# Optimization experiments

Measured on AMD Instinct MI355X. Metric: run time of the kernel, lower is better.

## Reference

```python
import jax, jax.numpy as jnp
import numpy as np

B, N, E = 256, 512, 8192
F_IN, DEPTH, NHID = 128, 3, 256
CAT = F_IN + DEPTH * NHID  # 896


def setup_inputs() -> dict:
    key = jax.random.key(0)
    ks = jax.random.split(key, 20)
    def w(k, shape, fan_in):
        return jax.random.normal(k, shape, jnp.float32) / np.sqrt(fan_in)
    inp = {
        "x": jax.random.normal(ks[0], (B, N, F_IN), jnp.float32),
        "edge_index": jax.random.randint(ks[1], (2, E), 0, N, jnp.int64),
        # linears: first maps F_IN->NHID, rest NHID->NHID (stacked)
        "lin0_W": w(ks[2], (F_IN, NHID), F_IN),
        "lin0_b": jnp.zeros((NHID,), jnp.float32),
        "lin_Ws": w(ks[3], (DEPTH - 1, NHID, NHID), NHID),
        "lin_bs": jnp.zeros((DEPTH - 1, NHID), jnp.float32),
        # GCNConv weights (stacked), PyG semantics: A_norm (X W) + b
        "conv_Ws": w(ks[4], (DEPTH, NHID, NHID), NHID),
        "conv_bs": jnp.zeros((DEPTH, NHID), jnp.float32),
        "sig_W": w(ks[5], (CAT, NHID), CAT),
        "sig_b": jnp.zeros((NHID,), jnp.float32),
        "tanh_W": w(ks[6], (CAT, NHID), CAT),
        "tanh_b": jnp.zeros((NHID,), jnp.float32),
        "f1_W": w(ks[7], (NHID, NHID), NHID),
        "f1_b": jnp.zeros((NHID,), jnp.float32),
        "f2_W": w(ks[8], (NHID, 2), NHID),
        "f2_b": jnp.zeros((2,), jnp.float32),
    }
    return inp


def _gcn_norm(edge_index, n):
    # add self loops, compute symmetric normalization D^-1/2 (A+I) D^-1/2
    loop = jnp.arange(n, dtype=edge_index.dtype)
    src = jnp.concatenate([edge_index[0], loop])
    dst = jnp.concatenate([edge_index[1], loop])
    deg = jax.ops.segment_sum(jnp.ones_like(src, jnp.float32), dst, num_segments=n)
    dinv = jax.lax.rsqrt(jnp.maximum(deg, 1.0))
    norm = dinv[src] * dinv[dst]  # [E+N]
    return src, dst, norm


def _gcn(h, W, b, src, dst, norm, n):
    # h: [B, N, C]
    hW = h @ W
    msg = hW[:, src, :] * norm[None, :, None]          # [B, E+N, C]
    agg = jax.vmap(lambda m: jax.ops.segment_sum(m, dst, num_segments=n))(msg)
    return agg + b


def reference(x, edge_index, lin0_W, lin0_b, lin_Ws, lin_bs, conv_Ws, conv_bs,
              sig_W, sig_b, tanh_W, tanh_b, f1_W, f1_b, f2_W, f2_b):
    n = x.shape[1]
    src, dst, norm = _gcn_norm(edge_index, n)
    xs = [x]
    out = x
    for i in range(DEPTH):
        if i == 0:
            out = out @ lin0_W + lin0_b
        else:
            out = out @ lin_Ws[i - 1] + lin_bs[i - 1]
        out = _gcn(out, conv_Ws[i], conv_bs[i], src, dst, norm, n)
        out = jnp.tanh(out)
        xs.append(out)
    cat = jnp.concatenate(xs, axis=-1)                 # [B, N, CAT]
    s = jax.nn.sigmoid(cat @ sig_W + sig_b)            # [B, N, NHID]
    t = jnp.tanh(cat @ tanh_W + tanh_b)                # [B, N, NHID]
    pooled = jnp.sum(s * t, axis=1)                    # [B, NHID] (sum over nodes)
    embeds = jnp.tanh(pooled)
    h = jax.nn.relu(embeds @ f1_W + f1_b)              # dropout is eval-mode identity
    preds = h @ f2_W + f2_b                            # [B, 2]
    preds = jnp.concatenate([jax.nn.sigmoid(preds[:, :1]), preds[:, 1:]], axis=-1)
    return preds, embeds
```

## Files before the change

### kernel.cpp

```cpp
#include <hip/hip_runtime.h>
#include <hip/hip_bf16.h>
#include <cstdint>

typedef _Float16 half_t;
typedef __attribute__((ext_vector_type(8))) _Float16 half8;
typedef __attribute__((ext_vector_type(4))) _Float16 half4;
typedef __attribute__((ext_vector_type(4))) float f32x4;

#define MFMA16x32(a, b, c) __builtin_amdgcn_mfma_f32_16x16x32_f16(a, b, c, 0, 0, 0)

static constexpr int NB  = 256;
static constexpr int NN  = 512;
static constexpr int NE  = 8192;
static constexpr int FIN = 128;
static constexpr int NH  = 256;
static constexpr int CAT = 896;

__device__ __forceinline__ void xcd_swz(int& bx, int& by)
{
    const int nwg = gridDim.x * gridDim.y;
    int wgid = blockIdx.y * gridDim.x + blockIdx.x;
    wgid = (wgid & 7) * (nwg >> 3) + (wgid >> 3);
    bx = wgid % gridDim.x;
    by = wgid / gridDim.x;
}

__device__ __forceinline__ void gload16(const half_t* __restrict__ g, half_t* l)
{
    __builtin_amdgcn_global_load_lds(
        (const __attribute__((address_space(1))) uint32_t*)(uintptr_t)g,
        (__attribute__((address_space(3))) uint32_t*)(uintptr_t)l, 16, 0, 0);
}

__device__ __forceinline__ void stage128x64(
    const half_t* __restrict__ src, long row0, int ldk, int k0,
    half_t* lds, int tid)
{
    const int wid = tid >> 6, lane = tid & 63;
#pragma unroll
    for (int it = 0; it < 4; ++it) {
        const int rb   = wid * 32 + it * 8;
        const int row  = rb + (lane >> 3);
        const int slot = (lane & 7) ^ (row & 7);
        gload16(src + (row0 + row) * (long)ldk + k0 + slot * 8,
                lds + (size_t)rb * 64);
    }
}

__device__ __forceinline__ half8 fragr(const half_t* lds, int row, int slot)
{
    return *(const half8*)(lds + row * 64 + ((slot ^ (row & 7)) * 8));
}

struct Tab {
    const void* src[16];
    float*      dst[16];
    int         n[16];
    int         fi[16];
    int         nseg;
};

__global__ void k_detect_all(Tab t, int* __restrict__ flags)
{
    const int s = blockIdx.x;
    if (s >= t.nseg) return;
    __shared__ int cnt_s;
    if (threadIdx.x == 0) cnt_s = 0;
    __syncthreads();
    const uint32_t* w = (const uint32_t*)t.src[s];
    int nw = t.n[s] / 2; if (nw > 2048) nw = 2048; if (nw < 1) nw = 1;
    int c = 0;
    for (int i = threadIdx.x; i < nw; i += 256) {
        const uint32_t lo = w[i] & 0xFFFFu;
        const int e = (int)((lo >> 7) & 0xFF);
        if (lo == 0u || (e >= 116 && e <= 136)) ++c;
    }
    atomicAdd(&cnt_s, c);
    __syncthreads();
    if (threadIdx.x == 0) flags[t.fi[s]] = (2 * cnt_s >= nw) ? 1 : 0;
}

__global__ void k_cvt_all(Tab t, const int* __restrict__ flags)
{
    for (int s = 0; s < t.nseg; ++s) {
        float* dst = t.dst[s];
        if (dst == nullptr) continue;
        const int is_bf = flags[t.fi[s]];
        const int n = t.n[s];
        const void* src = t.src[s];
        for (int i = blockIdx.x * 256 + threadIdx.x; i < n; i += gridDim.x * 256)
            dst[i] = is_bf
                ? __uint_as_float(((uint32_t)((const uint16_t*)src)[i]) << 16)
                : ((const float*)src)[i];
    }
}

__global__ void k_x2h(const void* __restrict__ xraw, half_t* __restrict__ o,
                      size_t n8, const int* __restrict__ flag)
{
    const int is_bf = *flag;
    const size_t gid0 = (size_t)blockIdx.x * blockDim.x + threadIdx.x;
    const size_t stride = (size_t)gridDim.x * blockDim.x;
    if (is_bf) {
        const uint4* src = (const uint4*)xraw;
        for (size_t i = gid0; i < n8; i += stride) {
            const uint4 v = src[i];
            half8 h;
            h[0] = (_Float16)__uint_as_float((v.x & 0xFFFFu) << 16);
            h[1] = (_Float16)__uint_as_float(v.x & 0xFFFF0000u);
            h[2] = (_Float16)__uint_as_float((v.y & 0xFFFFu) << 16);
            h[3] = (_Float16)__uint_as_float(v.y & 0xFFFF0000u);
            h[4] = (_Float16)__uint_as_float((v.z & 0xFFFFu) << 16);
            h[5] = (_Float16)__uint_as_float(v.z & 0xFFFF0000u);
            h[6] = (_Float16)__uint_as_float((v.w & 0xFFFFu) << 16);
            h[7] = (_Float16)__uint_as_float(v.w & 0xFFFF0000u);
            ((half8*)o)[i] = h;
        }
    } else {
        const float4* src = (const float4*)xraw;
        for (size_t i = gid0; i < n8; i += stride) {
            const float4 a = src[2 * i], b = src[2 * i + 1];
            half8 h;
            h[0] = (_Float16)a.x; h[1] = (_Float16)a.y;
            h[2] = (_Float16)a.z; h[3] = (_Float16)a.w;
            h[4] = (_Float16)b.x; h[5] = (_Float16)b.y;
            h[6] = (_Float16)b.z; h[7] = (_Float16)b.w;
            ((half8*)o)[i] = h;
        }
    }
}

__global__ void k_sentinel(__hip_bfloat16* __restrict__ out, float code)
{
    const int i = blockIdx.x * 256 + threadIdx.x;
    if (i < 66048) out[i] = __float2bfloat16(i < 512 ? code : 0.f);
}

__global__ void k_pick512(const float* __restrict__ a, const float* __restrict__ b,
                          float* __restrict__ f2Wc, float* __restrict__ linbsc)
{
    __shared__ float sa_s, sb_s;
    const int t = threadIdx.x;
    if (t == 0) { sa_s = 0.f; sb_s = 0.f; }
    __syncthreads();
    float va = fabsf(a[t]) + fabsf(a[t + 256]);
    float vb = fabsf(b[t]) + fabsf(b[t + 256]);
    for (int o = 32; o; o >>= 1) {
        va += __shfl_down(va, o, 64);
        vb += __shfl_down(vb, o, 64);
    }
    if ((t & 63) == 0) { atomicAdd(&sa_s, va); atomicAdd(&sb_s, vb); }
    __syncthreads();
    const float* f2 = (sa_s >= sb_s) ? a : b;
    const float* lb = (sa_s >= sb_s) ? b : a;
    f2Wc[t] = f2[t]; f2Wc[t + 256] = f2[t + 256];
    linbsc[t] = lb[t]; linbsc[t + 256] = lb[t + 256];
}

__global__ void k_build_graph(const int* __restrict__ ei, int* __restrict__ rowptr,
                              int* __restrict__ colx, float* __restrict__ wn,
                              float* __restrict__ srow)
{
    __shared__ int   degs[NN];
    __shared__ float dinv[NN];
    __shared__ int   rp[NN + 1];
    __shared__ int   cur[NN];
    __shared__ float sacc[NN];
    __shared__ int   is64_s;
    const int t = threadIdx.x;
    degs[t] = 0; cur[t] = 0; sacc[t] = 0.f;
    if (t == 0) {
        int orv = 0;
        for (int i = 1; i < 256; i += 2) orv |= ei[i];
        is64_s = (orv == 0) ? 1 : 0;
    }
    __syncthreads();
    const bool is64 = (is64_s != 0);
    auto EV = [&](int idx) { return is64 ? ei[2 * idx] : ei[idx]; };

    for (int e = t; e < NE; e += NN)
        atomicAdd(&degs[EV(NE + e)], 1);
    __syncthreads();
    const float dv = rsqrtf(fmaxf((float)(degs[t] + 1), 1.f));
    dinv[t] = dv;
    __syncthreads();
    if (t == 0) {
        rp[0] = 0;
        for (int i = 0; i < NN; ++i) rp[i + 1] = rp[i] + degs[i] + 1;
    }
    __syncthreads();
    rowptr[t] = rp[t];
    if (t == 0) rowptr[NN] = rp[NN];
    for (int e = t; e < NE; e += NN) {
        const int s = EV(e), d = EV(NE + e);
        const int pos = atomicAdd(&cur[d], 1);
        colx[rp[d] + pos] = s;
        wn[rp[d] + pos]   = dinv[s] * dinv[d];
        atomicAdd(&sacc[d], dinv[s]);
    }
    __syncthreads();
    const int slot = rp[t + 1] - 1;
    colx[slot] = t;
    wn[slot]   = dv * dv;
    srow[t]    = dv * (sacc[t] + dv);
}

__global__ void k_densify(const int* __restrict__ rowptr, const int* __restrict__ colx,
                          const float* __restrict__ wn, half_t* __restrict__ S16)
{
    __shared__ float row[NN];
    const int d = blockIdx.x;
    for (int i = threadIdx.x; i < NN; i += 256) row[i] = 0.f;
    __syncthreads();
    const int s0 = rowptr[d], s1 = rowptr[d + 1];
    for (int e = s0 + threadIdx.x; e < s1; e += 256)
        atomicAdd(&row[colx[e]], wn[e]);
    __syncthreads();
    for (int i = threadIdx.x; i < NN; i += 256)
        S16[(size_t)d * NN + i] = (half_t)row[i];
}

__global__ void k_fold_wc(const float* __restrict__ lin0_W, const float* __restrict__ lin_Ws,
                          const float* __restrict__ conv_Ws,
                          half_t* __restrict__ wc0, half_t* __restrict__ wc1,
                          half_t* __restrict__ wc2)
{
    const int layer = blockIdx.y;
    const int k = blockIdx.x;
    const int n = threadIdx.x;
    const int K = (layer == 0) ? FIN : NH;
    if (k >= K) return;
    const float* lin = (layer == 0) ? lin0_W : lin_Ws + (size_t)(layer - 1) * NH * NH;
    const float* cw  = conv_Ws + (size_t)layer * NH * NH;
    float s = 0.f;
    for (int j = 0; j < NH; ++j) s += lin[k * NH + j] * cw[j * NH + n];
    half_t* o = (layer == 0) ? wc0 : ((layer == 1) ? wc1 : wc2);
    o[n * K + k] = (half_t)s;
}

__global__ void k_fold_wt(const float* __restrict__ sigW, const float* __restrict__ tanW,
                          half_t* __restrict__ sh, half_t* __restrict__ th,
                          const float* __restrict__ lin0_b, const float* __restrict__ lin_bs,
                          const float* __restrict__ conv_Ws, float* __restrict__ vb)
{
    const int which = blockIdx.y;
    if (which == 2) {
        const int layer = blockIdx.x;
        if (layer >= 3) return;
        const int n = threadIdx.x;
        const float* lb = (layer == 0) ? lin0_b : lin_bs + (size_t)(layer - 1) * NH;
        const float* cw = conv_Ws + (size_t)layer * NH * NH;
        float s = 0.f;
        for (int j = 0; j < NH; ++j) s += lb[j] * cw[j * NH + n];
        vb[layer * NH + n] = s;
        return;
    }
    const int n = blockIdx.x;
    const float* W = which ? tanW : sigW;
    half_t* o = which ? th : sh;
    for (int k = threadIdx.x; k < CAT; k += 256)
        o[(size_t)n * CAT + k] = (half_t)W[(size_t)k * NH + n];
}

__global__ __launch_bounds__(256, 2) void k_gemm_t(
    const half_t* __restrict__ A, const half_t* __restrict__ BT,
    half_t* __restrict__ hwT, int K)
{
    __shared__ __align__(16) half_t sm[17408];
    half_t* lA = sm;
    half_t* lB = sm + 8192;
    int bx, by; xcd_swz(bx, by);
    const int tid = threadIdx.x;
    const int lane = tid & 63, wid = tid >> 6;
    const int wr = wid >> 1, wc = wid & 1;
    const int row_l = lane & 15, kg = lane >> 4;
    const long mbase = (long)bx * 128;
    const int nbase = by * 128;
    f32x4 acc[4][4] = {};
    for (int k0 = 0; k0 < K; k0 += 64) {
        stage128x64(A,  mbase, K, k0, lA, tid);
        stage128x64(BT, nbase, K, k0, lB, tid);
        __syncthreads();
#pragma unroll
        for (int ks = 0; ks < 2; ++ks) {
            half8 af[4], bf[4];
#pragma unroll
            for (int mt = 0; mt < 4; ++mt)
                af[mt] = fragr(lA, wr * 64 + mt * 16 + row_l, ks * 4 + kg);
#pragma unroll
            for (int nt = 0; nt < 4; ++nt)
                bf[nt] = fragr(lB, wc * 64 + nt * 16 + row_l, ks * 4 + kg);
#pragma unroll
            for (int mt = 0; mt < 4; ++mt)
#pragma unroll
                for (int nt = 0; nt < 4; ++nt)
                    acc[mt][nt] = MFMA16x32(af[mt], bf[nt], acc[mt][nt]);
        }
        __syncthreads();
    }
    half_t* lC = sm;
#pragma unroll
    for (int mt = 0; mt < 4; ++mt) {
        const int m_l = wr * 64 + mt * 16 + kg * 4;
#pragma unroll
        for (int nt = 0; nt < 4; ++nt) {
            const int n_l = wc * 64 + nt * 16 + row_l;
            half4 p;
            p[0] = (_Float16)acc[mt][nt][0]; p[1] = (_Float16)acc[mt][nt][1];
            p[2] = (_Float16)acc[mt][nt][2]; p[3] = (_Float16)acc[mt][nt][3];
            *(half4*)(lC + n_l * 136 + m_l) = p;
        }
    }
    __syncthreads();
    const int b  = (int)(mbase >> 9);
    const int s0 = (int)(mbase & 511);
#pragma unroll
    for (int pass = 0; pass < 8; ++pass) {
        const int n_l = pass * 16 + (tid >> 4);
        const int part = tid & 15;
        const half8 v = *(const half8*)(lC + n_l * 136 + part * 8);
        *(half8*)(hwT + ((size_t)b * 256 + nbase + n_l) * 512 + s0 + part * 8) = v;
    }
}

__global__ __launch_bounds__(256, 2) void k_gemm_agg(
    const half_t* __restrict__ S16, const half_t* __restrict__ hwT,
    const float* __restrict__ srow, const float* __restrict__ vb,
    const float* __restrict__ cb, half_t* __restrict__ hout)
{
    __shared__ __align__(16) half_t sm[17408];
    half_t* lA = sm;
    half_t* lB = sm + 8192;
    int bx, by; xcd_swz(bx, by);
    const int tid = threadIdx.x;
    const int lane = tid & 63, wid = tid >> 6;
    const int wr = wid >> 1, wc = wid & 1;
    const int row_l = lane & 15, kg = lane >> 4;
    const int mbase = bx * 128;
    const int nbase = by * 128;
    f32x4 acc[4][4] = {};
    for (int k0 = 0; k0 < 512; k0 += 64) {
        stage128x64(S16, mbase, 512, k0, lA, tid);
        stage128x64(hwT, nbase, 512, k0, lB, tid);
        __syncthreads();
#pragma unroll
        for (int ks = 0; ks < 2; ++ks) {
            half8 af[4], bf[4];
#pragma unroll
            for (int mt = 0; mt < 4; ++mt)
                af[mt] = fragr(lA, wr * 64 + mt * 16 + row_l, ks * 4 + kg);
#pragma unroll
            for (int nt = 0; nt < 4; ++nt)
                bf[nt] = fragr(lB, wc * 64 + nt * 16 + row_l, ks * 4 + kg);
#pragma unroll
            for (int mt = 0; mt < 4; ++mt)
#pragma unroll
                for (int nt = 0; nt < 4; ++nt)
                    acc[mt][nt] = MFMA16x32(af[mt], bf[nt], acc[mt][nt]);
        }
        __syncthreads();
    }
    const int b  = nbase >> 8;
    const int c0 = nbase & 255;
    half_t* lC = sm;
#pragma unroll
    for (int mt = 0; mt < 4; ++mt) {
        const int m_l = wr * 64 + mt * 16 + kg * 4;
        float sr[4];
#pragma unroll
        for (int r = 0; r < 4; ++r) sr[r] = srow[mbase + m_l + r];
#pragma unroll
        for (int nt = 0; nt < 4; ++nt) {
            const int n_l = wc * 64 + nt * 16 + row_l;
            const float vbc = vb[c0 + n_l], cbc = cb[c0 + n_l];
#pragma unroll
            for (int r = 0; r < 4; ++r)
                lC[(m_l + r) * 136 + n_l] =
                    (half_t)tanhf(acc[mt][nt][r] + sr[r] * vbc + cbc);
        }
    }
    __syncthreads();
#pragma unroll
    for (int pass = 0; pass < 8; ++pass) {
        const int row = pass * 16 + (tid >> 4);
        const int col = (tid & 15) * 8;
        const half8 v = *(const half8*)(lC + row * 136 + col);
        *(half8*)(hout + ((size_t)b * NN + mbase + row) * NH + c0 + col) = v;
    }
}

__global__ __launch_bounds__(256, 2) void k_gemm_final(
    const half_t* __restrict__ x16, const half_t* __restrict__ h1,
    const half_t* __restrict__ h2, const half_t* __restrict__ h3,
    const half_t* __restrict__ bsh, const half_t* __restrict__ bth,
    const float* __restrict__ sig_b, const float* __restrict__ tan_b,
    float* __restrict__ part)
{
    __shared__ __align__(16) half_t sm[24576];
    __shared__ float red[2][128];
    half_t* lA  = sm;
    half_t* lBs = sm + 8192;
    half_t* lBt = sm + 16384;
    int bx, by; xcd_swz(bx, by);
    const int tid = threadIdx.x;
    const int lane = tid & 63, wid = tid >> 6;
    const int wr = wid >> 1, wc = wid & 1;
    const int row_l = lane & 15, kg = lane >> 4;
    const long mbase = (long)bx * 128;
    const int sup = by;
    f32x4 aS[4][4] = {}, aT[4][4] = {};
    for (int kt = 0; kt < 14; ++kt) {
        const int k0 = kt * 64;
        const half_t* Aseg; int segK, lk;
        if (k0 < 128)      { Aseg = x16; segK = 128; lk = k0; }
        else if (k0 < 384) { Aseg = h1;  segK = 256; lk = k0 - 128; }
        else if (k0 < 640) { Aseg = h2;  segK = 256; lk = k0 - 384; }
        else               { Aseg = h3;  segK = 256; lk = k0 - 640; }
        stage128x64(Aseg, mbase, segK, lk, lA, tid);
        stage128x64(bsh, (long)sup * 128, CAT, k0, lBs, tid);
        stage128x64(bth, (long)sup * 128, CAT, k0, lBt, tid);
        __syncthreads();
#pragma unroll
        for (int ks = 0; ks < 2; ++ks) {
            half8 af[4];
#pragma unroll
            for (int mt = 0; mt < 4; ++mt)
                af[mt] = fragr(lA, wr * 64 + mt * 16 + row_l, ks * 4 + kg);
#pragma unroll
            for (int nt = 0; nt < 4; ++nt) {
                const int r = wc * 64 + nt * 16 + row_l;
                const half8 fs = fragr(lBs, r, ks * 4 + kg);
                const half8 ft = fragr(lBt, r, ks * 4 + kg);
#pragma unroll
                for (int mt = 0; mt < 4; ++mt) {
                    aS[mt][nt] = MFMA16x32(af[mt], fs, aS[mt][nt]);
                    aT[mt][nt] = MFMA16x32(af[mt], ft, aT[mt][nt]);
                }
            }
        }
        __syncthreads();
    }
#pragma unroll
    for (int nt = 0; nt < 4; ++nt) {
        const int j = sup * 128 + wc * 64 + nt * 16 + row_l;
        const float sb = sig_b[j], tb = tan_b[j];
        float ps = 0.f;
#pragma unroll
        for (int mt = 0; mt < 4; ++mt)
#pragma unroll
            for (int r = 0; r < 4; ++r) {
                const float u = aS[mt][nt][r] + sb;
                const float v = aT[mt][nt][r] + tb;
                ps += (1.f / (1.f + expf(-u))) * tanhf(v);
            }
        ps += __shfl_xor(ps, 16, 64);
        ps += __shfl_xor(ps, 32, 64);
        if (lane < 16) red[wr][wc * 64 + nt * 16 + lane] = ps;
    }
    __syncthreads();
    if (tid < 128)
        part[(long)bx * 256 + sup * 128 + tid] = red[0][tid] + red[1][tid];
}

__global__ __launch_bounds__(256) void k_finish(
    const float* __restrict__ part, const float* __restrict__ f1W,
    const float* __restrict__ f1b, const float* __restrict__ f2W,
    const float* __restrict__ f2b, void* __restrict__ dout,
    const int* __restrict__ flags)
{
    __shared__ float e[NH], h[NH];
    const int b = blockIdx.x, t = threadIdx.x;
    const int any = flags[0] | flags[1] | flags[2] | flags[3] | flags[4] |
                    flags[5] | flags[6];
    const int w4 = any ? 0 : 1;
    const float* p = part + (size_t)b * 1024 + t;
    const float ev = tanhf(p[0] + p[256] + p[512] + p[768]);
    e[t] = ev;
    if (w4) ((float*)dout)[512 + b * NH + t] = ev;
    else    ((__hip_bfloat16*)dout)[512 + b * NH + t] = __float2bfloat16(ev);
    __syncthreads();
    float a = f1b[t];
    for (int k = 0; k < NH; ++k) a += e[k] * f1W[k * NH + t];
    h[t] = fmaxf(a, 0.f);
    __syncthreads();
    if (t < 64) {
        float p0 = 0.f, p1 = 0.f;
        for (int jj = t; jj < NH; jj += 64) {
            p0 += h[jj] * f2W[jj * 2 + 0];
            p1 += h[jj] * f2W[jj * 2 + 1];
        }
        for (int o = 32; o; o >>= 1) {
            p0 += __shfl_down(p0, o, 64);
            p1 += __shfl_down(p1, o, 64);
        }
        if (t == 0) {
            p0 += f2b[0]; p1 += f2b[1];
            p0 = 1.f / (1.f + expf(-p0));
            if (w4) {
                ((float*)dout)[b * 2 + 0] = p0;
                ((float*)dout)[b * 2 + 1] = p1;
            } else {
                ((__hip_bfloat16*)dout)[b * 2 + 0] = __float2bfloat16(p0);
                ((__hip_bfloat16*)dout)[b * 2 + 1] = __float2bfloat16(p1);
            }
        }
    }
}

extern "C" void kernel_launch(void* const* d_in, const int* in_sizes, int n_in,
                              void* d_out, int out_size, void* d_ws, size_t ws_size,
                              hipStream_t stream)
{
    (void)out_size;

    int ix = -1, ie = -1, il0 = -1, ilw = -1, icw = -1, icb = -1, if1 = -1, if2b = -1;
    int i229[2] = {-1, -1}; int n229 = 0;
    int i512[2] = {-1, -1}; int n512 = 0;
    int i256[4] = {-1, -1, -1, -1}; int n256 = 0;
    int bad = 0;
    for (int i = 0; i < n_in && i < 16; ++i) {
        switch (in_sizes[i]) {
            case 16777216: ix = i; break;
            case 16384:    ie = i; break;
            case 32768:    il0 = i; break;
            case 131072:   ilw = i; break;
            case 196608:   icw = i; break;
            case 768:      icb = i; break;
            case 65536:    if1 = i; break;
            case 2:        if2b = i; break;
            case 229376:   if (n229 < 2) i229[n229++] = i; else bad = 1; break;
            case 512:      if (n512 < 2) i512[n512++] = i; else bad = 1; break;
            case 256:      if (n256 < 4) i256[n256++] = i; else bad = 1; break;
            default:       bad = 1; break;
        }
    }
    if (n_in != 16 || bad || ix < 0 || ie < 0 || il0 < 0 || ilw < 0 || icw < 0 ||
        icb < 0 || if1 < 0 || if2b < 0 || n229 != 2 || n512 != 2 || n256 != 4) {
        k_sentinel<<<(66048 + 255) / 256, 256, 0, stream>>>((__hip_bfloat16*)d_out, 20480.f);
        return;
    }

    char* wp = (char*)d_ws;
    auto alloc = [&](size_t sz) {
        char* p = wp;
        wp += (sz + 4095) & ~(size_t)4095;
        return p;
    };
    int*   flags  = (int*)alloc(32 * 4);
    float* c_lin0W  = (float*)alloc((size_t)FIN * NH * 4);
    float* c_linWs  = (float*)alloc((size_t)2 * NH * NH * 4);
    float* c_convWs = (float*)alloc((size_t)3 * NH * NH * 4);
    float* c_convbs = (float*)alloc((size_t)3 * NH * 4);
    float* c_sigW   = (float*)alloc((size_t)CAT * NH * 4);
    float* c_tanW   = (float*)alloc((size_t)CAT * NH * 4);
    float* c_f1W    = (float*)alloc((size_t)NH * NH * 4);
    float* c_f2b    = (float*)alloc(2 * 4);
    float* c_512a   = (float*)alloc(512 * 4);
    float* c_512b   = (float*)alloc(512 * 4);
    float* f2Wc     = (float*)alloc(512 * 4);
    float* linbsc   = (float*)alloc(512 * 4);
    float* c_b256[4];
    for (int q = 0; q < 4; ++q) c_b256[q] = (float*)alloc(256 * 4);
    int*    rowptr = (int*)alloc((NN + 1) * 4);
    int*    colx   = (int*)alloc((NE + NN) * 4);
    float*  wn     = (float*)alloc((NE + NN) * 4);
    float*  srow   = (float*)alloc(NN * 4);
    float*  vb     = (float*)alloc(3 * NH * 4);
    half_t* S16  = (half_t*)alloc((size_t)NN * NN * 2);
    half_t* wc0  = (half_t*)alloc((size_t)NH * FIN * 2);
    half_t* wc1  = (half_t*)alloc((size_t)NH * NH * 2);
    half_t* wc2  = (half_t*)alloc((size_t)NH * NH * 2);
    half_t* sgh  = (half_t*)alloc((size_t)NH * CAT * 2);
    half_t* tnh  = (half_t*)alloc((size_t)NH * CAT * 2);
    float*  part = (float*)alloc((size_t)1024 * 256 * 4);
    half_t* x16  = (half_t*)alloc((size_t)NB * NN * FIN * 2);

    const size_t fixed_end = (size_t)(wp - (char*)d_ws);
    int CB = 256;
    while (CB > 4) {
        const size_t mc = (size_t)CB * NN;
        const size_t act = 4 * ((mc * NH * 2 + 4095) & ~(size_t)4095);
        if (fixed_end + act + (1u << 20) <= ws_size) break;
        CB >>= 1;
    }
    const size_t MC = (size_t)CB * NN;
    const int NCH = NB / CB;

    half_t* h1c  = (half_t*)alloc(MC * NH * 2);
    half_t* h2c  = (half_t*)alloc(MC * NH * 2);
    half_t* h3c  = (half_t*)alloc(MC * NH * 2);
    half_t* hwT  = (half_t*)alloc(MC * NH * 2);

    Tab t = {};
    int s = 0;
    auto addseg = [&](int idx, float* dst, int n, int fi) {
        t.src[s] = d_in[idx]; t.dst[s] = dst; t.n[s] = n; t.fi[s] = fi; ++s;
    };
    addseg(ix,      nullptr,   16777216, 0);
    addseg(il0,     c_lin0W,   FIN * NH, 1);
    addseg(ilw,     c_linWs,   2 * NH * NH, 2);
    addseg(icw,     c_convWs,  3 * NH * NH, 3);
    addseg(i229[0], c_sigW,    CAT * NH, 4);
    addseg(i229[1], c_tanW,    CAT * NH, 5);
    addseg(if1,     c_f1W,     NH * NH, 6);
    addseg(i512[0], c_512a,    512, 7);
    addseg(i512[1], c_512b,    512, 8);
    for (int q = 0; q < 4; ++q) addseg(i256[q], c_b256[q], 256, 9 + q);
    addseg(icb,     c_convbs,  3 * NH, 13);
    addseg(if2b,    c_f2b,     2, 14);
    t.nseg = s;

    k_detect_all<<<t.nseg, 256, 0, stream>>>(t, flags);
    k_cvt_all<<<1024, 256, 0, stream>>>(t, flags);
    k_pick512<<<1, 256, 0, stream>>>(c_512a, c_512b, f2Wc, linbsc);

    const float* lin0_b = c_b256[0];
    const float* sig_b  = c_b256[1];
    const float* tan_b  = c_b256[2];
    const float* f1_b   = c_b256[3];

    k_build_graph<<<1, 512, 0, stream>>>((const int*)d_in[ie], rowptr, colx, wn, srow);
    k_densify<<<NN, 256, 0, stream>>>(rowptr, colx, wn, S16);
    k_fold_wc<<<dim3(256, 3), 256, 0, stream>>>(c_lin0W, c_linWs, c_convWs, wc0, wc1, wc2);
    k_fold_wt<<<dim3(256, 3), 256, 0, stream>>>(c_sigW, c_tanW, sgh, tnh,
                                                lin0_b, linbsc, c_convWs, vb);
    k_x2h<<<2048, 256, 0, stream>>>(d_in[ix], x16, (size_t)NB * NN * FIN / 8, flags + 0);

    for (int c = 0; c < NCH; ++c) {
        half_t* x16c = x16 + (size_t)c * MC * FIN;
        k_gemm_t<<<dim3(CB * 4, 2), 256, 0, stream>>>(x16c, wc0, hwT, 128);
        k_gemm_agg<<<dim3(4, CB * 2), 256, 0, stream>>>(S16, hwT, srow, vb + 0,
                                                        c_convbs + 0, h1c);
        k_gemm_t<<<dim3(CB * 4, 2), 256, 0, stream>>>(h1c, wc1, hwT, 256);
        k_gemm_agg<<<dim3(4, CB * 2), 256, 0, stream>>>(S16, hwT, srow, vb + 256,
                                                        c_convbs + 256, h2c);
        k_gemm_t<<<dim3(CB * 4, 2), 256, 0, stream>>>(h2c, wc2, hwT, 256);
        k_gemm_agg<<<dim3(4, CB * 2), 256, 0, stream>>>(S16, hwT, srow, vb + 512,
                                                        c_convbs + 512, h3c);
        k_gemm_final<<<dim3(CB * 4, 2), 256, 0, stream>>>(
            x16c, h1c, h2c, h3c, sgh, tnh, sig_b, tan_b,
            part + (size_t)c * CB * 1024);
    }
    k_finish<<<NB, 256, 0, stream>>>(part, c_f1W, f1_b, f2Wc, c_f2b, d_out, flags);
}
```

Baseline: 514.5 us.

## Double-buffer LDS in GEMMs, enlarge final GEMM tile, split chunking

The transform and aggregation GEMMs now double-buffer their LDS tiles, so the next k-slice is staged while the current one is consumed, with one barrier per iteration instead of two. The final sig/tanh GEMM now runs 512 threads over 256-row tiles, which halves the partial-sum buffer and the reduction work in k_finish. Host chunking keeps h1..h3 for a larger batch chunk, so the final GEMM launches fewer times while the layer GEMMs run in sub-chunks of up to 128 graphs. The extra LDS (64KB per block) may lower occupancy relative to the two blocks per CU requested by the launch bounds.

```diff
diff --git a/kernel.cpp b/kernel.cpp
--- a/kernel.cpp
+++ b/kernel.cpp
@@ -266,9 +266,7 @@
     const half_t* __restrict__ A, const half_t* __restrict__ BT,
     half_t* __restrict__ hwT, int K)
 {
-    __shared__ __align__(16) half_t sm[17408];
-    half_t* lA = sm;
-    half_t* lB = sm + 8192;
+    __shared__ __align__(16) half_t sm[32768];
     int bx, by; xcd_swz(bx, by);
     const int tid = threadIdx.x;
     const int lane = tid & 63, wid = tid >> 6;
@@ -276,25 +274,32 @@
     const int row_l = lane & 15, kg = lane >> 4;
     const long mbase = (long)bx * 128;
     const int nbase = by * 128;
+    const int nt = K >> 6;
     f32x4 acc[4][4] = {};
-    for (int k0 = 0; k0 < K; k0 += 64) {
-        stage128x64(A,  mbase, K, k0, lA, tid);
-        stage128x64(BT, nbase, K, k0, lB, tid);
-        __syncthreads();
+    stage128x64(A,  mbase, K, 0, sm, tid);
+    stage128x64(BT, nbase, K, 0, sm + 8192, tid);
+    __syncthreads();
+    for (int kt = 0; kt < nt; ++kt) {
+        half_t* cur = sm + (kt & 1) * 16384;
+        if (kt + 1 < nt) {
+            half_t* nxt = sm + ((kt + 1) & 1) * 16384;
+            stage128x64(A,  mbase, K, (kt + 1) * 64, nxt, tid);
+            stage128x64(BT, nbase, K, (kt + 1) * 64, nxt + 8192, tid);
+        }
 #pragma unroll
         for (int ks = 0; ks < 2; ++ks) {
             half8 af[4], bf[4];
 #pragma unroll
             for (int mt = 0; mt < 4; ++mt)
-                af[mt] = fragr(lA, wr * 64 + mt * 16 + row_l, ks * 4 + kg);
-#pragma unroll
-            for (int nt = 0; nt < 4; ++nt)
-                bf[nt] = fragr(lB, wc * 64 + nt * 16 + row_l, ks * 4 + kg);
+                af[mt] = fragr(cur, wr * 64 + mt * 16 + row_l, ks * 4 + kg);
+#pragma unroll
+            for (int ntc = 0; ntc < 4; ++ntc)
+                bf[ntc] = fragr(cur + 8192, wc * 64 + ntc * 16 + row_l, ks * 4 + kg);
 #pragma unroll
             for (int mt = 0; mt < 4; ++mt)
 #pragma unroll
-                for (int nt = 0; nt < 4; ++nt)
-                    acc[mt][nt] = MFMA16x32(af[mt], bf[nt], acc[mt][nt]);
+                for (int ntc = 0; ntc < 4; ++ntc)
+                    acc[mt][ntc] = MFMA16x32(af[mt], bf[ntc], acc[mt][ntc]);
         }
         __syncthreads();
     }
@@ -303,11 +308,11 @@
     for (int mt = 0; mt < 4; ++mt) {
         const int m_l = wr * 64 + mt * 16 + kg * 4;
 #pragma unroll
-        for (int nt = 0; nt < 4; ++nt) {
-            const int n_l = wc * 64 + nt * 16 + row_l;
+        for (int ntc = 0; ntc < 4; ++ntc) {
+            const int n_l = wc * 64 + ntc * 16 + row_l;
             half4 p;
-            p[0] = (_Float16)acc[mt][nt][0]; p[1] = (_Float16)acc[mt][nt][1];
-            p[2] = (_Float16)acc[mt][nt][2]; p[3] = (_Float16)acc[mt][nt][3];
+            p[0] = (_Float16)acc[mt][ntc][0]; p[1] = (_Float16)acc[mt][ntc][1];
+            p[2] = (_Float16)acc[mt][ntc][2]; p[3] = (_Float16)acc[mt][ntc][3];
             *(half4*)(lC + n_l * 136 + m_l) = p;
         }
     }
@@ -328,9 +333,7 @@
     const float* __restrict__ srow, const float* __restrict__ vb,
     const float* __restrict__ cb, half_t* __restrict__ hout)
 {
-    __shared__ __align__(16) half_t sm[17408];
-    half_t* lA = sm;
-    half_t* lB = sm + 8192;
+    __shared__ __align__(16) half_t sm[32768];
     int bx, by; xcd_swz(bx, by);
     const int tid = threadIdx.x;
     const int lane = tid & 63, wid = tid >> 6;
@@ -339,24 +342,30 @@
     const int mbase = bx * 128;
     const int nbase = by * 128;
     f32x4 acc[4][4] = {};
-    for (int k0 = 0; k0 < 512; k0 += 64) {
-        stage128x64(S16, mbase, 512, k0, lA, tid);
-        stage128x64(hwT, nbase, 512, k0, lB, tid);
-        __syncthreads();
+    stage128x64(S16, mbase, 512, 0, sm, tid);
+    stage128x64(hwT, nbase, 512, 0, sm + 8192, tid);
+    __syncthreads();
+    for (int kt = 0; kt < 8; ++kt) {
+        half_t* cur = sm + (kt & 1) * 16384;
+        if (kt + 1 < 8) {
+            half_t* nxt = sm + ((kt + 1) & 1) * 16384;
+            stage128x64(S16, mbase, 512, (kt + 1) * 64, nxt, tid);
+            stage128x64(hwT, nbase, 512, (kt + 1) * 64, nxt + 8192, tid);
+        }
 #pragma unroll
         for (int ks = 0; ks < 2; ++ks) {
             half8 af[4], bf[4];
 #pragma unroll
             for (int mt = 0; mt < 4; ++mt)
-                af[mt] = fragr(lA, wr * 64 + mt * 16 + row_l, ks * 4 + kg);
-#pragma unroll
-            for (int nt = 0; nt < 4; ++nt)
-                bf[nt] = fragr(lB, wc * 64 + nt * 16 + row_l, ks * 4 + kg);
+                af[mt] = fragr(cur, wr * 64 + mt * 16 + row_l, ks * 4 + kg);
+#pragma unroll
+            for (int ntc = 0; ntc < 4; ++ntc)
+                bf[ntc] = fragr(cur + 8192, wc * 64 + ntc * 16 + row_l, ks * 4 + kg);
 #pragma unroll
             for (int mt = 0; mt < 4; ++mt)
 #pragma unroll
-                for (int nt = 0; nt < 4; ++nt)
-                    acc[mt][nt] = MFMA16x32(af[mt], bf[nt], acc[mt][nt]);
+                for (int ntc = 0; ntc < 4; ++ntc)
+                    acc[mt][ntc] = MFMA16x32(af[mt], bf[ntc], acc[mt][ntc]);
         }
         __syncthreads();
     }
@@ -370,13 +379,13 @@
 #pragma unroll
         for (int r = 0; r < 4; ++r) sr[r] = srow[mbase + m_l + r];
 #pragma unroll
-        for (int nt = 0; nt < 4; ++nt) {
-            const int n_l = wc * 64 + nt * 16 + row_l;
+        for (int ntc = 0; ntc < 4; ++ntc) {
+            const int n_l = wc * 64 + ntc * 16 + row_l;
             const float vbc = vb[c0 + n_l], cbc = cb[c0 + n_l];
 #pragma unroll
             for (int r = 0; r < 4; ++r)
                 lC[(m_l + r) * 136 + n_l] =
-                    (half_t)tanhf(acc[mt][nt][r] + sr[r] * vbc + cbc);
+                    (half_t)tanhf(acc[mt][ntc][r] + sr[r] * vbc + cbc);
         }
     }
     __syncthreads();
@@ -389,24 +398,22 @@
     }
 }
 
-__global__ __launch_bounds__(256, 2) void k_gemm_final(
+__global__ __launch_bounds__(512) void k_gemm_final(
     const half_t* __restrict__ x16, const half_t* __restrict__ h1,
     const half_t* __restrict__ h2, const half_t* __restrict__ h3,
     const half_t* __restrict__ bsh, const half_t* __restrict__ bth,
     const float* __restrict__ sig_b, const float* __restrict__ tan_b,
     float* __restrict__ part)
 {
-    __shared__ __align__(16) half_t sm[24576];
-    __shared__ float red[2][128];
-    half_t* lA  = sm;
-    half_t* lBs = sm + 8192;
-    half_t* lBt = sm + 16384;
+    __shared__ __align__(16) half_t lA[16384];
+    __shared__ __align__(16) half_t lBs[8192], lBt[8192];
+    __shared__ float red[4][128];
     int bx, by; xcd_swz(bx, by);
     const int tid = threadIdx.x;
     const int lane = tid & 63, wid = tid >> 6;
     const int wr = wid >> 1, wc = wid & 1;
     const int row_l = lane & 15, kg = lane >> 4;
-    const long mbase = (long)bx * 128;
+    const long mbase = (long)bx * 256;
     const int sup = by;
     f32x4 aS[4][4] = {}, aT[4][4] = {};
     for (int kt = 0; kt < 14; ++kt) {
@@ -416,9 +423,24 @@
         else if (k0 < 384) { Aseg = h1;  segK = 256; lk = k0 - 128; }
         else if (k0 < 640) { Aseg = h2;  segK = 256; lk = k0 - 384; }
         else               { Aseg = h3;  segK = 256; lk = k0 - 640; }
-        stage128x64(Aseg, mbase, segK, lk, lA, tid);
-        stage128x64(bsh, (long)sup * 128, CAT, k0, lBs, tid);
-        stage128x64(bth, (long)sup * 128, CAT, k0, lBt, tid);
+#pragma unroll
+        for (int it = 0; it < 4; ++it) {
+            const int rb   = it * 64 + wid * 8;
+            const int row  = rb + (lane >> 3);
+            const int slot = (lane & 7) ^ (row & 7);
+            gload16(Aseg + (mbase + row) * (long)segK + lk + slot * 8,
+                    lA + (size_t)rb * 64);
+        }
+#pragma unroll
+        for (int it = 0; it < 2; ++it) {
+            const int rb   = it * 64 + wid * 8;
+            const int row  = rb + (lane >> 3);
+            const int slot = (lane & 7) ^ (row & 7);
+            gload16(bsh + ((long)sup * 128 + row) * CAT + k0 + slot * 8,
+                    lBs + (size_t)rb * 64);
+            gload16(bth + ((long)sup * 128 + row) * CAT + k0 + slot * 8,
+                    lBt + (size_t)rb * 64);
+        }
         __syncthreads();
 #pragma unroll
         for (int ks = 0; ks < 2; ++ks) {
@@ -427,39 +449,40 @@
             for (int mt = 0; mt < 4; ++mt)
                 af[mt] = fragr(lA, wr * 64 + mt * 16 + row_l, ks * 4 + kg);
 #pragma unroll
-            for (int nt = 0; nt < 4; ++nt) {
-                const int r = wc * 64 + nt * 16 + row_l;
+            for (int ntc = 0; ntc < 4; ++ntc) {
+                const int r = wc * 64 + ntc * 16 + row_l;
                 const half8 fs = fragr(lBs, r, ks * 4 + kg);
                 const half8 ft = fragr(lBt, r, ks * 4 + kg);
 #pragma unroll
                 for (int mt = 0; mt < 4; ++mt) {
-                    aS[mt][nt] = MFMA16x32(af[mt], fs, aS[mt][nt]);
-                    aT[mt][nt] = MFMA16x32(af[mt], ft, aT[mt][nt]);
+                    aS[mt][ntc] = MFMA16x32(af[mt], fs, aS[mt][ntc]);
+                    aT[mt][ntc] = MFMA16x32(af[mt], ft, aT[mt][ntc]);
                 }
             }
         }
         __syncthreads();
     }
 #pragma unroll
-    for (int nt = 0; nt < 4; ++nt) {
-        const int j = sup * 128 + wc * 64 + nt * 16 + row_l;
+    for (int ntc = 0; ntc < 4; ++ntc) {
+        const int j = sup * 128 + wc * 64 + ntc * 16 + row_l;
         const float sb = sig_b[j], tb = tan_b[j];
         float ps = 0.f;
 #pragma unroll
         for (int mt = 0; mt < 4; ++mt)
 #pragma unroll
             for (int r = 0; r < 4; ++r) {
-                const float u = aS[mt][nt][r] + sb;
-                const float v = aT[mt][nt][r] + tb;
+                const float u = aS[mt][ntc][r] + sb;
+                const float v = aT[mt][ntc][r] + tb;
                 ps += (1.f / (1.f + expf(-u))) * tanhf(v);
             }
         ps += __shfl_xor(ps, 16, 64);
         ps += __shfl_xor(ps, 32, 64);
-        if (lane < 16) red[wr][wc * 64 + nt * 16 + lane] = ps;
+        if (lane < 16) red[wr][wc * 64 + ntc * 16 + lane] = ps;
     }
     __syncthreads();
     if (tid < 128)
-        part[(long)bx * 256 + sup * 128 + tid] = red[0][tid] + red[1][tid];
+        part[(size_t)(bx >> 1) * 512 + (bx & 1) * 256 + sup * 128 + tid] =
+            red[0][tid] + red[1][tid] + red[2][tid] + red[3][tid];
 }
 
 __global__ __launch_bounds__(256) void k_finish(
@@ -473,8 +496,8 @@
     const int any = flags[0] | flags[1] | flags[2] | flags[3] | flags[4] |
                     flags[5] | flags[6];
     const int w4 = any ? 0 : 1;
-    const float* p = part + (size_t)b * 1024 + t;
-    const float ev = tanhf(p[0] + p[256] + p[512] + p[768]);
+    const float* p = part + (size_t)b * 512 + t;
+    const float ev = tanhf(p[0] + p[256]);
     e[t] = ev;
     if (w4) ((float*)dout)[512 + b * NH + t] = ev;
     else    ((__hip_bfloat16*)dout)[512 + b * NH + t] = __float2bfloat16(ev);
@@ -572,24 +595,23 @@
     half_t* wc2  = (half_t*)alloc((size_t)NH * NH * 2);
     half_t* sgh  = (half_t*)alloc((size_t)NH * CAT * 2);
     half_t* tnh  = (half_t*)alloc((size_t)NH * CAT * 2);
-    float*  part = (float*)alloc((size_t)1024 * 256 * 4);
+    float*  part = (float*)alloc((size_t)NB * 512 * 4);
     half_t* x16  = (half_t*)alloc((size_t)NB * NN * FIN * 2);
 
     const size_t fixed_end = (size_t)(wp - (char*)d_ws);
-    int CB = 256;
-    while (CB > 4) {
-        const size_t mc = (size_t)CB * NN;
-        const size_t act = 4 * ((mc * NH * 2 + 4095) & ~(size_t)4095);
-        if (fixed_end + act + (1u << 20) <= ws_size) break;
-        CB >>= 1;
-    }
-    const size_t MC = (size_t)CB * NN;
-    const int NCH = NB / CB;
-
-    half_t* h1c  = (half_t*)alloc(MC * NH * 2);
-    half_t* h2c  = (half_t*)alloc(MC * NH * 2);
-    half_t* h3c  = (half_t*)alloc(MC * NH * 2);
-    half_t* hwT  = (half_t*)alloc(MC * NH * 2);
+    int CBF = 256;
+    int CBL;
+    for (;;) {
+        CBL = (CBF < 128) ? CBF : 128;
+        const size_t hbytes  = 3 * (((size_t)CBF * NN * NH * 2 + 4095) & ~(size_t)4095);
+        const size_t hwbytes = (((size_t)CBL * NN * NH * 2 + 4095) & ~(size_t)4095);
+        if (fixed_end + hbytes + hwbytes + (1u << 20) <= ws_size || CBF <= 8) break;
+        CBF >>= 1;
+    }
+    half_t* h1  = (half_t*)alloc((size_t)CBF * NN * NH * 2);
+    half_t* h2  = (half_t*)alloc((size_t)CBF * NN * NH * 2);
+    half_t* h3  = (half_t*)alloc((size_t)CBF * NN * NH * 2);
+    half_t* hwT = (half_t*)alloc((size_t)CBL * NN * NH * 2);
 
     Tab t = {};
     int s = 0;
@@ -626,20 +648,26 @@
                                                 lin0_b, linbsc, c_convWs, vb);
     k_x2h<<<2048, 256, 0, stream>>>(d_in[ix], x16, (size_t)NB * NN * FIN / 8, flags + 0);
 
-    for (int c = 0; c < NCH; ++c) {
-        half_t* x16c = x16 + (size_t)c * MC * FIN;
-        k_gemm_t<<<dim3(CB * 4, 2), 256, 0, stream>>>(x16c, wc0, hwT, 128);
-        k_gemm_agg<<<dim3(4, CB * 2), 256, 0, stream>>>(S16, hwT, srow, vb + 0,
-                                                        c_convbs + 0, h1c);
-        k_gemm_t<<<dim3(CB * 4, 2), 256, 0, stream>>>(h1c, wc1, hwT, 256);
-        k_gemm_agg<<<dim3(4, CB * 2), 256, 0, stream>>>(S16, hwT, srow, vb + 256,
-                                                        c_convbs + 256, h2c);
-        k_gemm_t<<<dim3(CB * 4, 2), 256, 0, stream>>>(h2c, wc2, hwT, 256);
-        k_gemm_agg<<<dim3(4, CB * 2), 256, 0, stream>>>(S16, hwT, srow, vb + 512,
-                                                        c_convbs + 512, h3c);
-        k_gemm_final<<<dim3(CB * 4, 2), 256, 0, stream>>>(
-            x16c, h1c, h2c, h3c, sgh, tnh, sig_b, tan_b,
-            part + (size_t)c * CB * 1024);
+    const int NFC = NB / CBF;
+    const int NLC = CBF / CBL;
+    for (int fc = 0; fc < NFC; ++fc) {
+        for (int lc = 0; lc < NLC; ++lc) {
+            const size_t goff = (size_t)(fc * CBF + lc * CBL);
+            half_t* x16c = x16 + goff * NN * FIN;
+            const size_t hoff = (size_t)lc * CBL * NN * NH;
+            k_gemm_t<<<dim3(CBL * 4, 2), 256, 0, stream>>>(x16c, wc0, hwT, 128);
+            k_gemm_agg<<<dim3(4, CBL * 2), 256, 0, stream>>>(S16, hwT, srow, vb + 0,
+                                                             c_convbs + 0, h1 + hoff);
+            k_gemm_t<<<dim3(CBL * 4, 2), 256, 0, stream>>>(h1 + hoff, wc1, hwT, 256);
+            k_gemm_agg<<<dim3(4, CBL * 2), 256, 0, stream>>>(S16, hwT, srow, vb + 256,
+                                                             c_convbs + 256, h2 + hoff);
+            k_gemm_t<<<dim3(CBL * 4, 2), 256, 0, stream>>>(h2 + hoff, wc2, hwT, 256);
+            k_gemm_agg<<<dim3(4, CBL * 2), 256, 0, stream>>>(S16, hwT, srow, vb + 512,
+                                                             c_convbs + 512, h3 + hoff);
+        }
+        k_gemm_final<<<dim3(CBF * 2, 2), 512, 0, stream>>>(
+            x16 + (size_t)fc * CBF * NN * FIN, h1, h2, h3, sgh, tnh,
+            sig_b, tan_b, part + (size_t)fc * CBF * 512);
     }
     k_finish<<<NB, 256, 0, stream>>>(part, c_f1W, f1_b, f2Wc, c_f2b, d_out, flags);
 }
```

Measured after the change: 564.0 us. +9.6%, slower.
